# Kernel optimization log

Measured on AMD Instinct MI355X. Metric: run time of the kernel, lower is better.

Reference implementation:

```python
import jax, jax.numpy as jnp
import numpy as np

N, E = 3200, 50000
RBF, HID = 16, 128
CUT = 5.0
NS, NV = 32, 16            # multiplicities of 0e and 1o blocks
D = NS + 3 * NV            # 80 = node/message irrep dim
WNUM = NS*NS + NV*NS + NS*NV + NV*NV  # 2304 tensor-product weights per edge
EPS = 1e-8
# path normalization (fully-connected TP, 2 paths per output irrep)
A1 = 1.0 / np.sqrt(2.0 * NS)
A2 = 1.0 / np.sqrt(2.0 * NV)
A3 = 1.0 / np.sqrt(2.0 * NS)
A4 = 1.0 / np.sqrt(2.0 * NV)
ISQ3 = 1.0 / np.sqrt(3.0)


def setup_inputs() -> dict:
    key = jax.random.key(0)
    ks = jax.random.split(key, 24)
    nrm = lambda k, s, sc=1.0: jax.random.normal(k, s, jnp.float32) * sc
    x = nrm(ks[0], (N, D))
    edge_src = jax.random.randint(ks[1], (E,), 0, N)
    edge_dst = jax.random.randint(ks[2], (E,), 0, N)
    dirs = nrm(ks[3], (E, 3))
    unit = dirs / jnp.linalg.norm(dirs, axis=1, keepdims=True)
    # component-normalized SH for l=0,1: [1, sqrt(3)*r_hat]
    edge_sh = jnp.concatenate([jnp.ones((E, 1), jnp.float32), np.sqrt(3.0) * unit], axis=1)
    edge_rbf = nrm(ks[4], (E, RBF))
    edge_len = jax.random.uniform(ks[5], (E,), jnp.float32, 0.1, 6.0)  # some beyond cutoff
    inp = dict(x=x, edge_src=edge_src, edge_dst=edge_dst, edge_sh=edge_sh,
               edge_rbf=edge_rbf, edge_len=edge_len)
    # IrrepNorm affine params
    inp['norm_w'] = jnp.ones((D,), jnp.float32)
    inp['norm_b'] = jnp.zeros((D,), jnp.float32)
    # radial weight MLP (RBF -> HID -> HID -> WNUM)
    inp['mw1'] = nrm(ks[6], (RBF, HID), 1.0/np.sqrt(RBF)); inp['mb1'] = jnp.zeros((HID,), jnp.float32)
    inp['mw2'] = nrm(ks[7], (HID, HID), 1.0/np.sqrt(HID)); inp['mb2'] = jnp.zeros((HID,), jnp.float32)
    inp['mw3'] = nrm(ks[8], (HID, WNUM), 1.0/np.sqrt(HID)); inp['mb3'] = jnp.zeros((WNUM,), jnp.float32)
    # edge gate MLP (RBF -> HID -> 1)
    inp['gw1'] = nrm(ks[9], (RBF, HID), 1.0/np.sqrt(RBF)); inp['gb1'] = jnp.zeros((HID,), jnp.float32)
    inp['gw2'] = nrm(ks[10], (HID, 1), 1.0/np.sqrt(HID)); inp['gb2'] = jnp.zeros((1,), jnp.float32)
    # equivariant linears (e3nn stores N(0,1) weights, normalizes by 1/sqrt(fan_in))
    inp['Ws'] = nrm(ks[11], (NS, NS + NV))   # msg_linear scalar part: 32 -> 32 scalars + 16 gates
    inp['Wv'] = nrm(ks[12], (NV, NV))        # msg_linear vector part
    inp['Us'] = nrm(ks[13], (NS, NS))        # update_linear
    inp['Uv'] = nrm(ks[14], (NV, NV))
    inp['Ss'] = nrm(ks[15], (NS, NS))        # self_linear
    inp['Sv'] = nrm(ks[16], (NV, NV))
    inp['res_scale'] = jnp.float32(0.1)
    return inp


def _irrep_norm(x, w, b):
    s = x[:, :NS]
    v = x[:, NS:].reshape(-1, NV, 3)
    mean = s.mean(axis=1, keepdims=True)
    var = ((s - mean) ** 2).mean(axis=1, keepdims=True)
    s = (s - mean) / jnp.sqrt(var + EPS)
    rms = jnp.sqrt((v ** 2).mean(axis=2, keepdims=True) + EPS)
    v = v / rms
    out = jnp.concatenate([s, v.reshape(-1, 3 * NV)], axis=-1)
    return out * w + b


def reference(x, edge_src, edge_dst, edge_sh, edge_rbf, edge_len,
              norm_w, norm_b, mw1, mb1, mw2, mb2, mw3, mb3,
              gw1, gb1, gw2, gb2, Ws, Wv, Us, Uv, Ss, Sv, res_scale):
    silu = jax.nn.silu
    x_norm = _irrep_norm(x, norm_w, norm_b)                  # [N, 80]
    # radial tensor-product weights per edge
    h = silu(edge_rbf @ mw1 + mb1)
    h = silu(h @ mw2 + mb2)
    tpw = h @ mw3 + mb3                                      # [E, 2304]
    o1 = NS*NS; o2 = o1 + NV*NS; o3 = o2 + NS*NV
    w1 = tpw[:, :o1].reshape(-1, NS, NS)
    w2 = tpw[:, o1:o2].reshape(-1, NV, NS)
    w3 = tpw[:, o2:o3].reshape(-1, NS, NV)
    w4 = tpw[:, o3:].reshape(-1, NV, NV)
    # gather source node features
    xs = x_norm[edge_src, :NS]                               # [E, 32]
    xv = x_norm[edge_src, NS:].reshape(-1, NV, 3)            # [E, 16, 3]
    sh0 = edge_sh[:, 0]                                      # [E]
    sh1 = edge_sh[:, 1:4]                                    # [E, 3]
    # fully-connected TP paths
    msg_s = A1 * jnp.einsum('ei,eio->eo', xs * sh0[:, None], w1)
    inner = jnp.einsum('eim,em->ei', xv, sh1) * ISQ3         # 1o x 1o -> 0e
    msg_s = msg_s + A2 * jnp.einsum('ei,eio->eo', inner, w2)
    msg_v = A3 * jnp.einsum('ei,eio->eo', xs, w3)[:, :, None] * sh1[:, None, :]
    msg_v = msg_v + A4 * jnp.einsum('eim,eio->eom', xv, w4) * sh0[:, None, None]
    m = jnp.concatenate([msg_s, msg_v.reshape(-1, 3 * NV)], axis=-1)  # [E, 80]
    # cutoff envelope and learned edge gate
    cutoff_w = 0.5 * (jnp.cos(jnp.pi * edge_len / CUT) + 1.0) * (edge_len <= CUT).astype(x.dtype)
    gate_w = jax.nn.sigmoid(silu(edge_rbf @ gw1 + gb1) @ gw2 + gb2)   # [E, 1]
    edge_w = cutoff_w[:, None] * gate_w                               # [E, 1]
    m = m * edge_w
    # scatter-add aggregate + normalization
    agg = jax.ops.segment_sum(m, edge_dst, num_segments=N)            # [N, 80]
    den = jax.ops.segment_sum(edge_w, edge_dst, num_segments=N)       # [N, 1]
    agg = agg / jnp.maximum(den, 1e-8)
    # msg_linear -> scalars + gates + gated vectors
    ag_s = agg[:, :NS]
    ag_v = agg[:, NS:].reshape(-1, NV, 3)
    sc = (ag_s @ Ws) / np.sqrt(NS)                                    # [N, 48]
    vc = jnp.einsum('nim,io->nom', ag_v, Wv) / np.sqrt(NV)            # [N, 16, 3]
    s_g = silu(sc[:, :NS])
    gates = jax.nn.sigmoid(sc[:, NS:])
    v_g = vc * gates[:, :, None]
    # update + self interaction
    upd_s = (s_g @ Us) / np.sqrt(NS)
    upd_v = jnp.einsum('nim,io->nom', v_g, Uv) / np.sqrt(NV)
    self_s = (x_norm[:, :NS] @ Ss) / np.sqrt(NS)
    self_v = jnp.einsum('nim,io->nom', x_norm[:, NS:].reshape(-1, NV, 3), Sv) / np.sqrt(NV)
    out = jnp.concatenate([self_s + upd_s, (self_v + upd_v).reshape(-1, 3 * NV)], axis=-1)
    return x + res_scale * out
```

## Files before the change

kernel.cpp:

```cpp
#include <hip/hip_runtime.h>
#include <hip/hip_bf16.h>
#include <math.h>

#define N_NODES 3200
#define E_EDGES 50000
#define RBFN 16
#define HID 128
#define NS 32
#define NV 16
#define DD 80
#define WNUM 2304
#define CUTF 5.0f
#define EPSF 1e-8f

#define A1C 0.125f
#define A2C 0.17677669529663687f
#define A3C 0.125f
#define A4C 0.17677669529663687f
#define A2ISQ 0.10206207261596575f

typedef __attribute__((ext_vector_type(4))) float f32x4;
typedef __attribute__((ext_vector_type(8))) short bf16x8;

__device__ __forceinline__ float sigm(float x) { return 1.0f / (1.0f + __expf(-x)); }
__device__ __forceinline__ float silu_f(float x) { return x * sigm(x); }

__device__ __forceinline__ short bf16r(float x) {
    union { float f; unsigned u; } v; v.f = x;
    unsigned r = (v.u + 0x7fffu + ((v.u >> 16) & 1u)) >> 16;
    return (short)r;
}
__device__ __forceinline__ float b2f(unsigned short s) {
    union { float f; unsigned u; } v; v.u = ((unsigned)s) << 16; return v.f;
}

__global__ __launch_bounds__(256) void k_pre(
    const int* __restrict__ edst, int* __restrict__ start,
    const float* __restrict__ mw2, __hip_bfloat16* __restrict__ mw2f,
    const float* __restrict__ mw3, const float* __restrict__ mb3,
    __hip_bfloat16* __restrict__ mw3f, __hip_bfloat16* __restrict__ biasf,
    const float* __restrict__ x, const float* __restrict__ nw, const float* __restrict__ nb,
    float* __restrict__ xn, unsigned short* __restrict__ xnb) {
    __shared__ __align__(16) char sm[16640];
    int b = blockIdx.x, t = threadIdx.x;
    if (b == 0) {
        int* histl = (int*)sm;
        int* part  = (int*)(sm + 12800);
        for (int i = t; i < N_NODES; i += 256) histl[i] = 0;
        __syncthreads();
        for (int i = t; i < E_EDGES; i += 256) atomicAdd(&histl[edst[i]], 1);
        __syncthreads();
        int loc[13];
        int s = 0;
#pragma unroll
        for (int j = 0; j < 13; j++) {
            int idx = t * 13 + j;
            int v = (idx < N_NODES) ? histl[idx] : 0;
            loc[j] = s; s += v;
        }
        part[t] = s;
        __syncthreads();
        for (int off = 1; off < 256; off <<= 1) {
            int v = part[t];
            int add = (t >= off) ? part[t - off] : 0;
            __syncthreads();
            part[t] = v + add;
            __syncthreads();
        }
        int pre = (t == 0) ? 0 : part[t - 1];
#pragma unroll
        for (int j = 0; j < 13; j++) {
            int idx = t * 13 + j;
            if (idx < N_NODES) start[idx] = pre + loc[j];
        }
        if (t == 255) start[N_NODES] = part[255];
    } else if (b < 9) {
        __hip_bfloat16* st = (__hip_bfloat16*)sm;
        int tt = b - 1;
        for (int idx = t; idx < 2048; idx += 256) {
            int k = idx >> 4, c = idx & 15;
            float v = mw2[k * HID + tt * 16 + c];
            int kk = k >> 5, q4 = (k >> 3) & 3, j = k & 7;
            st[kk * 512 + (q4 * 16 + c) * 8 + j] = __float2bfloat16(v);
        }
        __syncthreads();
        ((bf16x8*)(mw2f + tt * 2048))[t] = ((const bf16x8*)st)[t];
    } else if (b < 154) {
        int b2 = b - 9;
        __hip_bfloat16* st = (__hip_bfloat16*)sm;
        if (b2 < 144) {
            for (int idx = t; idx < 2048; idx += 256) {
                int k = idx >> 4, c = idx & 15;
                float v = mw3[k * WNUM + b2 * 16 + c];
                int kk = k >> 5, q4 = (k >> 3) & 3, j = k & 7;
                st[kk * 512 + (q4 * 16 + c) * 8 + j] = __float2bfloat16(v);
            }
            __syncthreads();
            ((bf16x8*)(mw3f + b2 * 2048))[t] = ((const bf16x8*)st)[t];
        } else {
            for (int idx = t; idx < 3072; idx += 256) {
                float val;
                if (idx < 1024) {
                    int oh = idx >> 9, l = (idx >> 3) & 63, j = idx & 7;
                    int o = oh * 16 + (l & 15), i = (l >> 4) * 8 + j;
                    val = mb3[i * 32 + o];
                } else if (idx < 2048) {
                    int tt = idx - 1024;
                    int oh = tt >> 9, l = (tt >> 3) & 63, j = tt & 7;
                    int o = oh * 16 + (l & 15), i = (l >> 4) * 8 + j;
                    val = (i < 16) ? mb3[1024 + i * 32 + o] : 0.f;
                } else if (idx < 2560) {
                    int tt = idx - 2048;
                    int l = tt >> 3, j = tt & 7;
                    int o = l & 15, i = (l >> 4) * 8 + j;
                    val = mb3[1536 + i * 16 + o];
                } else {
                    int tt = idx - 2560;
                    int l = tt >> 3, j = tt & 7;
                    int o = l & 15, i = (l >> 4) * 8 + j;
                    val = (i < 16) ? mb3[2048 + i * 16 + o] : 0.f;
                }
                biasf[idx] = __float2bfloat16(val);
            }
        }
    } else {
        float* row = (float*)sm;
        int sub = t >> 6, tt = t & 63;
        int n = (b - 154) * 4 + sub;
        float* rw = row + sub * 80;
        const float* xr = x + n * DD;
        rw[tt] = xr[tt];
        if (tt < 16) rw[64 + tt] = xr[64 + tt];
        __syncthreads();
        float mean = 0.f;
#pragma unroll
        for (int i = 0; i < NS; i++) mean += rw[i];
        mean *= (1.0f / NS);
        float var = 0.f;
#pragma unroll
        for (int i = 0; i < NS; i++) { float d = rw[i] - mean; var += d * d; }
        var *= (1.0f / NS);
        float inv_ = rsqrtf(var + EPSF);
        if (tt < NS) {
            float v = (rw[tt] - mean) * inv_ * nw[tt] + nb[tt];
            xn[n * DD + tt] = v;
            xnb[n * DD + tt] = (unsigned short)bf16r(v);
        }
        if (tt < 48) {
            int j = tt / 3;
            float v0 = rw[NS + 3 * j], v1 = rw[NS + 3 * j + 1], v2 = rw[NS + 3 * j + 2];
            float rms = sqrtf((v0 * v0 + v1 * v1 + v2 * v2) * (1.0f / 3.0f) + EPSF);
            float v = rw[NS + tt] / rms * nw[NS + tt] + nb[NS + tt];
            xn[n * DD + NS + tt] = v;
            xnb[n * DD + NS + tt] = (unsigned short)bf16r(v);
        }
    }
}

__global__ void k_scatter(const int* __restrict__ edst, const int* __restrict__ esrc,
                          const float* __restrict__ esh, const int* __restrict__ start,
                          int* __restrict__ cur, int* __restrict__ inv,
                          int* __restrict__ edstp, int* __restrict__ esrcp,
                          float* __restrict__ eshp) {
    int e = blockIdx.x * 256 + threadIdx.x;
    if (e < E_EDGES) {
        int d = edst[e];
        int pos = start[d] + atomicAdd(&cur[d], 1);
        inv[e] = pos;
        edstp[pos] = d;
        esrcp[pos] = esrc[e];
        f32x4 s = *(const f32x4*)(esh + e * 4);
        *(f32x4*)(eshp + pos * 4) = s;
    }
}

__global__ __launch_bounds__(256) void k_front(
    const float* __restrict__ rbf, const float* __restrict__ elen,
    const int* __restrict__ inv,
    const float* __restrict__ mw1, const float* __restrict__ mb1,
    const float* __restrict__ gw1, const float* __restrict__ gb1,
    const float* __restrict__ gw2, const float* __restrict__ gb2,
    const float* __restrict__ mb2, const __hip_bfloat16* __restrict__ mw2f,
    float* __restrict__ ewg, unsigned short* __restrict__ h2p) {
    __shared__ __align__(16) char smem[16640];
    int b = blockIdx.x, tid = threadIdx.x;
    __hip_bfloat16* h1l = (__hip_bfloat16*)smem;
    float* gatep = (float*)(smem + 16384);
    int wid = __builtin_amdgcn_readfirstlane(tid >> 6);
    int lane = tid & 63;
    int base = b * 64;
    int eb = base + wid * 16;
    {
        int c0 = lane, c1 = 64 + lane;
        float t0[16], t1[16], g0[16], g1[16];
        float b0 = mb1[c0], b1 = mb1[c1], gb0v = gb1[c0], gb1v = gb1[c1];
#pragma unroll
        for (int e = 0; e < 16; e++) { t0[e] = b0; t1[e] = b1; g0[e] = gb0v; g1[e] = gb1v; }
#pragma unroll
        for (int r = 0; r < RBFN; r++) {
            float w0 = mw1[r * HID + c0], w1 = mw1[r * HID + c1];
            float v0 = gw1[r * HID + c0], v1 = gw1[r * HID + c1];
#pragma unroll
            for (int e = 0; e < 16; e++) {
                int ee = eb + e; if (ee >= E_EDGES) ee = E_EDGES - 1;
                float rv = rbf[ee * RBFN + r];
                t0[e] += rv * w0; t1[e] += rv * w1;
                g0[e] += rv * v0; g1[e] += rv * v1;
            }
        }
        float q0 = gw2[c0], q1 = gw2[c1];
        float gb2v = gb2[0];
#pragma unroll
        for (int e = 0; e < 16; e++) {
            int le = wid * 16 + e;
            h1l[le * 128 + c0] = __float2bfloat16(silu_f(t0[e]));
            h1l[le * 128 + c1] = __float2bfloat16(silu_f(t1[e]));
            float p = silu_f(g0[e]) * q0 + silu_f(g1[e]) * q1;
            p += __shfl_xor(p, 1);  p += __shfl_xor(p, 2);  p += __shfl_xor(p, 4);
            p += __shfl_xor(p, 8);  p += __shfl_xor(p, 16); p += __shfl_xor(p, 32);
            if (lane == 0) gatep[le] = p + gb2v;
        }
    }
    __syncthreads();
    if (lane < 16) {
        int ee = eb + lane;
        if (ee < E_EDGES) {
            float len = elen[ee];
            float cut = (len <= CUTF) ? 0.5f * (cosf(3.14159265358979f * len / CUTF) + 1.0f) : 0.f;
            ewg[inv[ee]] = cut * sigm(gatep[wid * 16 + lane]);
        }
    }
    {
        int q4 = lane >> 4, l15 = lane & 15;
        int le = wid * 16 + l15;
        bf16x8 af[4];
#pragma unroll
        for (int kk = 0; kk < 4; kk++)
            af[kk] = *(const bf16x8*)(h1l + le * 128 + kk * 32 + q4 * 8);
        int pos4[4];
#pragma unroll
        for (int r = 0; r < 4; r++) {
            int ge = base + wid * 16 + q4 * 4 + r;
            pos4[r] = (ge < E_EDGES) ? inv[ge] : -1;
        }
        const f32x4 zf = {0.f, 0.f, 0.f, 0.f};
#pragma unroll
        for (int ct = 0; ct < 8; ct++) {
            f32x4 acc = zf;
#pragma unroll
            for (int kk = 0; kk < 4; kk++) {
                bf16x8 bw = *(const bf16x8*)(mw2f + (ct * 4 + kk) * 512 + lane * 8);
                acc = __builtin_amdgcn_mfma_f32_16x16x32_bf16(af[kk], bw, acc, 0, 0, 0);
            }
            float bias = mb2[ct * 16 + l15];
            int c = ct * 16 + l15;
            int f = c >> 3, j = c & 7;
#pragma unroll
            for (int r = 0; r < 4; r++) {
                int pos = pos4[r];
                if (pos >= 0)
                    h2p[(pos >> 4) * 2048 + f * 128 + (pos & 15) * 8 + j] =
                        (unsigned short)bf16r(silu_f(acc[r] + bias));
            }
        }
    }
}

__global__ __launch_bounds__(128, 2) void k_msg(
    const unsigned short* __restrict__ xnb, const unsigned short* __restrict__ h2p,
    const float* __restrict__ ewg, const int* __restrict__ edstp,
    const int* __restrict__ esrcp, const float* __restrict__ eshp,
    const __hip_bfloat16* __restrict__ mw3f, const __hip_bfloat16* __restrict__ biasf,
    const int* __restrict__ startp, float* __restrict__ agg, float* __restrict__ agg2,
    float* __restrict__ den) {
    __shared__ __align__(16) char pool[30720];
    unsigned short (*xng)[88]  = (unsigned short(*)[88])(pool);
    unsigned short (*innr)[16] = (unsigned short(*)[16])(pool + 22528);
    float* sh0l = (float*)(pool + 26624);
    int* srcl   = (int*)(pool + 27136);
    int* dstl   = (int*)(pool + 27648);
    float* ewl  = (float*)(pool + 28160);
    float (*sh1l)[4] = (float(*)[4])(pool + 28672);
    float* msgl = (float*)pool;

    const int tid = threadIdx.x;
    const int wid = __builtin_amdgcn_readfirstlane(tid >> 6);
    const int lane = tid & 63;
    const int q4 = lane >> 4;
    const int l15 = lane & 15;
    const int ib = q4 * 8;
    const int xcd = blockIdx.x & 7;
    const int j8 = blockIdx.x >> 3;
    const int grp = xcd + 8 * (j8 / 5);
    const int slice = j8 - 5 * (j8 / 5);
    if (grp >= 391) return;
    const int e0 = grp * 128;

    {
        int slot = e0 + tid;
        bool v = slot < E_EDGES;
        dstl[tid] = v ? edstp[slot] : -1;
        srcl[tid] = v ? esrcp[slot] : 0;
        ewl[tid]  = v ? ewg[slot] : 0.f;
        f32x4 s = {0.f, 0.f, 0.f, 0.f};
        if (v) s = *(const f32x4*)(eshp + slot * 4);
        sh0l[tid] = s[0];
        sh1l[tid][0] = s[1]; sh1l[tid][1] = s[2]; sh1l[tid][2] = s[3];
    }
    __syncthreads();
    if (slice < 2) {
        for (int idx = tid; idx < 128 * 4; idx += 128) {
            int e = idx >> 2, q = (idx & 3) * 8;
            *(bf16x8*)&xng[e][q] = *(const bf16x8*)(xnb + srcl[e] * 80 + q);
        }
    } else if (slice < 4) {
        for (int idx = tid; idx < 128 * 7; idx += 128) {
            int e = idx / 7, q = 24 + (idx - e * 7) * 8;
            *(bf16x8*)&xng[e][q] = *(const bf16x8*)(xnb + srcl[e] * 80 + q);
        }
    } else {
        for (int idx = tid; idx < 128 * 10; idx += 128) {
            int e = idx / 10, q = (idx - e * 10) * 8;
            *(bf16x8*)&xng[e][q] = *(const bf16x8*)(xnb + srcl[e] * 80 + q);
        }
    }
    __syncthreads();
    if (slice == 2 || slice == 3) {
        for (int idx = tid; idx < 128 * 16; idx += 128) {
            int e = idx >> 4, i = idx & 15;
            float d = b2f(xng[e][32 + 3 * i]) * sh1l[e][0]
                    + b2f(xng[e][32 + 3 * i + 1]) * sh1l[e][1]
                    + b2f(xng[e][32 + 3 * i + 2]) * sh1l[e][2];
            innr[e][i] = (unsigned short)bf16r(A2ISQ * d);
        }
        __syncthreads();
    }

    int el[4];
#pragma unroll
    for (int et = 0; et < 4; et++) el[et] = wid * 64 + et * 16 + l15;
    const int tbase = (e0 >> 4) + wid * 4;
    bf16x8 hfr[4][4];
#pragma unroll
    for (int et = 0; et < 4; et++) {
        const unsigned short* tp = h2p + (tbase + et) * 2048;
#pragma unroll
        for (int kk = 0; kk < 4; kk++)
            hfr[et][kk] = *(const bf16x8*)(tp + (kk * 4 + q4) * 128 + l15 * 8);
    }
    const f32x4 zf = {0.f, 0.f, 0.f, 0.f};
    const bf16x8* gp = (const bf16x8*)mw3f;
    int cnt = E_EDGES - e0; if (cnt > 128) cnt = 128;

    if (slice < 4) {
        const int h = slice & 1;
        const int ch2 = slice >> 1;
        const int nlo = ch2 * 24, nhi = nlo + 24;
        float f1[4];
        f32x4 msgS[4];
#pragma unroll
        for (int et = 0; et < 4; et++) f1[et] = A1C * sh0l[el[et]];
#pragma unroll
        for (int et = 0; et < 4; et++) {
            bf16x8 pb;
            if (ch2 == 0) {
#pragma unroll
                for (int j = 0; j < 8; j++)
                    pb[j] = bf16r(b2f(xng[el[et]][ib + j]) * f1[et]);
            } else {
#pragma unroll
                for (int j = 0; j < 8; j++)
                    pb[j] = (ib + j < 16) ? (short)innr[el[et]][ib + j] : (short)0;
            }
            bf16x8 ba = *(const bf16x8*)(biasf + (ch2 * 1024 + h * 512) + lane * 8);
            msgS[et] = __builtin_amdgcn_mfma_f32_16x16x32_bf16(ba, pb, zf, 0, 0, 0);
        }
        auto computeS = [&](int n, bf16x8 (&A)[4]) {
            f32x4 acc[4];
#pragma unroll
            for (int et = 0; et < 4; et++) acc[et] = zf;
#pragma unroll
            for (int kk = 0; kk < 4; kk++)
#pragma unroll
                for (int et = 0; et < 4; et++)
                    acc[et] = __builtin_amdgcn_mfma_f32_16x16x32_bf16(
                        A[kk], hfr[et][kk], acc[et], 0, 0, 0);
            float p[4];
            if (n < 32) {
#pragma unroll
                for (int et = 0; et < 4; et++) p[et] = f1[et] * b2f(xng[el[et]][n]);
            } else {
#pragma unroll
                for (int et = 0; et < 4; et++) p[et] = b2f(innr[el[et]][n - 32]);
            }
#pragma unroll
            for (int et = 0; et < 4; et++)
#pragma unroll
                for (int r = 0; r < 4; r++)
                    msgS[et][r] += p[et] * acc[et][r];
        };
        bf16x8 A0[4], A1[4];
        {
            const bf16x8* g = gp + nlo * 512 + h * 256;
#pragma unroll
            for (int f = 0; f < 4; f++) A0[f] = g[f * 64 + lane];
        }
        for (int n = nlo; n < nhi; n += 2) {
            const bf16x8* g1 = gp + (n + 1) * 512 + h * 256;
#pragma unroll
            for (int f = 0; f < 4; f++) A1[f] = g1[f * 64 + lane];
            computeS(n, A0);
            if (n + 2 < nhi) {
                const bf16x8* g2 = gp + (n + 2) * 512 + h * 256;
#pragma unroll
                for (int f = 0; f < 4; f++) A0[f] = g2[f * 64 + lane];
            }
            computeS(n + 1, A1);
        }
        __syncthreads();
#pragma unroll
        for (int et = 0; et < 4; et++) {
            int le = el[et];
            float ew = ewl[le];
#pragma unroll
            for (int r = 0; r < 4; r++)
                msgl[le * 16 + q4 * 4 + r] = msgS[et][r] * ew;
        }
        __syncthreads();
        {
            int nch = (slice == 0) ? 17 : 16;
            int c = lane;
            int r0 = wid * 64;
            int rend = (cnt < r0 + 64) ? cnt : (r0 + 64);
            if (c < nch && r0 < cnt) {
                int cur = dstl[r0];
                float acc = 0.f;
                for (int r = r0; r < rend; r++) {
                    int nd = dstl[r];
                    if (nd != cur) {
                        if (cur >= 0) {
                            bool interior = (startp[cur] >= e0 + r0) && (startp[cur + 1] <= e0 + rend);
                            float* p = (c == 16) ? (den + cur)
                                     : ((slice == 0) ? (agg + cur * 80 + c)
                                     :  (slice == 1) ? (agg + cur * 80 + 16 + c)
                                     :  (slice == 2) ? (agg2 + cur * 32 + c)
                                                     : (agg2 + cur * 32 + 16 + c));
                            if (interior) *p = acc; else atomicAdd(p, acc);
                        }
                        acc = 0.f; cur = nd;
                    }
                    acc += (c == 16) ? ewl[r] : msgl[r * 16 + c];
                }
                if (cur >= 0) {
                    bool interior = (startp[cur] >= e0 + r0) && (startp[cur + 1] <= e0 + rend);
                    float* p = (c == 16) ? (den + cur)
                             : ((slice == 0) ? (agg + cur * 80 + c)
                             :  (slice == 1) ? (agg + cur * 80 + 16 + c)
                             :  (slice == 2) ? (agg2 + cur * 32 + c)
                                             : (agg2 + cur * 32 + 16 + c));
                    if (interior) *p = acc; else atomicAdd(p, acc);
                }
            }
        }
    } else {
        float f4e[4];
#pragma unroll
        for (int et = 0; et < 4; et++) f4e[et] = A4C * sh0l[el[et]];
        f32x4 q3[4];
#pragma unroll
        for (int et = 0; et < 4; et++) {
            bf16x8 xs8;
#pragma unroll
            for (int j = 0; j < 8; j++) xs8[j] = (short)xng[el[et]][ib + j];
            bf16x8 ba3 = *(const bf16x8*)(biasf + 2048 + lane * 8);
            q3[et] = __builtin_amdgcn_mfma_f32_16x16x32_bf16(ba3, xs8, zf, 0, 0, 0);
        }
        for (int n = 48; n < 64; ++n) {
            bf16x8 A[8];
            const bf16x8* g = gp + n * 512;
#pragma unroll
            for (int f = 0; f < 8; f++) A[f] = g[f * 64 + lane];
#pragma unroll
            for (int half = 0; half < 2; half++) {
                f32x4 acc[4];
#pragma unroll
                for (int et = 0; et < 4; et++) acc[et] = zf;
#pragma unroll
                for (int kk = 0; kk < 4; kk++)
#pragma unroll
                    for (int et = 0; et < 4; et++)
                        acc[et] = __builtin_amdgcn_mfma_f32_16x16x32_bf16(
                            A[half * 4 + kk], hfr[et][kk], acc[et], 0, 0, 0);
                int i = 2 * (n - 48) + half;
                float p[4];
#pragma unroll
                for (int et = 0; et < 4; et++) p[et] = b2f(xng[el[et]][i]);
#pragma unroll
                for (int et = 0; et < 4; et++)
#pragma unroll
                    for (int r = 0; r < 4; r++)
                        q3[et][r] += p[et] * acc[et][r];
            }
        }
        f32x4 qv[3][4];
#pragma unroll
        for (int et = 0; et < 4; et++) {
            bf16x8 ba4 = *(const bf16x8*)(biasf + 2560 + lane * 8);
#pragma unroll
            for (int m = 0; m < 3; m++) {
                bf16x8 t8;
#pragma unroll
                for (int j = 0; j < 8; j++) {
                    int i = ib + j;
                    t8[j] = (i < 16) ? (short)xng[el[et]][32 + 3 * i + m] : (short)0;
                }
                qv[m][et] = __builtin_amdgcn_mfma_f32_16x16x32_bf16(ba4, t8, zf, 0, 0, 0);
            }
        }
        for (int n = 64; n < 72; ++n) {
            bf16x8 A[8];
            const bf16x8* g = gp + n * 512;
#pragma unroll
            for (int f = 0; f < 8; f++) A[f] = g[f * 64 + lane];
#pragma unroll
            for (int half = 0; half < 2; half++) {
                f32x4 acc[4];
#pragma unroll
                for (int et = 0; et < 4; et++) acc[et] = zf;
#pragma unroll
                for (int kk = 0; kk < 4; kk++)
#pragma unroll
                    for (int et = 0; et < 4; et++)
                        acc[et] = __builtin_amdgcn_mfma_f32_16x16x32_bf16(
                            A[half * 4 + kk], hfr[et][kk], acc[et], 0, 0, 0);
                int i = 2 * (n - 64) + half;
#pragma unroll
                for (int m = 0; m < 3; m++) {
                    float p[4];
#pragma unroll
                    for (int et = 0; et < 4; et++) p[et] = b2f(xng[el[et]][32 + 3 * i + m]);
#pragma unroll
                    for (int et = 0; et < 4; et++)
#pragma unroll
                        for (int r = 0; r < 4; r++)
                            qv[m][et][r] += p[et] * acc[et][r];
                }
            }
        }
        __syncthreads();
#pragma unroll
        for (int et = 0; et < 4; et++) {
            int le = el[et];
            float ew = ewl[le];
            float s0 = sh1l[le][0], s1 = sh1l[le][1], s2 = sh1l[le][2];
            float b4 = f4e[et];
#pragma unroll
            for (int r = 0; r < 4; r++) {
                int o = q4 * 4 + r;
                float qq = A3C * q3[et][r];
                msgl[le * 48 + o * 3 + 0] = (qq * s0 + b4 * qv[0][et][r]) * ew;
                msgl[le * 48 + o * 3 + 1] = (qq * s1 + b4 * qv[1][et][r]) * ew;
                msgl[le * 48 + o * 3 + 2] = (qq * s2 + b4 * qv[2][et][r]) * ew;
            }
        }
        __syncthreads();
        {
            int c = lane;
            int r0 = wid * 64;
            int rend = (cnt < r0 + 64) ? cnt : (r0 + 64);
            if (c < 48 && r0 < cnt) {
                int cur = dstl[r0];
                float acc = 0.f;
                for (int r = r0; r < rend; r++) {
                    int nd = dstl[r];
                    if (nd != cur) {
                        if (cur >= 0) {
                            bool interior = (startp[cur] >= e0 + r0) && (startp[cur + 1] <= e0 + rend);
                            float* p = agg + cur * 80 + 32 + c;
                            if (interior) *p = acc; else atomicAdd(p, acc);
                        }
                        acc = 0.f; cur = nd;
                    }
                    acc += msgl[r * 48 + c];
                }
                if (cur >= 0) {
                    bool interior = (startp[cur] >= e0 + r0) && (startp[cur + 1] <= e0 + rend);
                    float* p = agg + cur * 80 + 32 + c;
                    if (interior) *p = acc; else atomicAdd(p, acc);
                }
            }
        }
    }
}

__global__ __launch_bounds__(256) void k_update(
    const float* __restrict__ x, const float* __restrict__ xn,
    const float* __restrict__ agg, const float* __restrict__ agg2,
    const float* __restrict__ den,
    const float* __restrict__ Ws, const float* __restrict__ Wv,
    const float* __restrict__ Us, const float* __restrict__ Uv,
    const float* __restrict__ Ss, const float* __restrict__ Sv,
    const float* __restrict__ rsp, float* __restrict__ out) {
    int sub = threadIdx.x >> 6, t = threadIdx.x & 63;
    int n = blockIdx.x * 4 + sub;
    __shared__ float ag[4][DD];
    __shared__ float xnl[4][DD];
    __shared__ float sg[4][NS];
    __shared__ float gt[4][NV];
    __shared__ float vg[4][48];
    float idv = 1.0f / fmaxf(den[n], 1e-8f);
    float base = agg[n * DD + t];
    if (t < 32) base += agg2[n * 32 + t];
    ag[sub][t] = base * idv;
    if (t < 16) ag[sub][64 + t] = agg[n * DD + 64 + t] * idv;
    xnl[sub][t] = xn[n * DD + t];
    if (t < 16) xnl[sub][64 + t] = xn[n * DD + 64 + t];
    __syncthreads();
    const float iqs = 0.17677669529663687f;
    const float iqv = 0.25f;
    if (t < 48) {
        float acc = 0.f;
#pragma unroll
        for (int i = 0; i < NS; i++) acc += ag[sub][i] * Ws[i * 48 + t];
        acc *= iqs;
        if (t < NS) sg[sub][t] = silu_f(acc);
        else gt[sub][t - NS] = sigm(acc);
    }
    __syncthreads();
    if (t < 48) {
        int o = t / 3, m = t - 3 * o;
        float acc = 0.f;
#pragma unroll
        for (int i = 0; i < NV; i++) acc += ag[sub][NS + 3 * i + m] * Wv[i * NV + o];
        vg[sub][t] = acc * iqv * gt[sub][o];
    }
    __syncthreads();
    float rs = rsp[0];
    if (t < NS) {
        float us = 0.f, ss = 0.f;
#pragma unroll
        for (int i = 0; i < NS; i++) { us += sg[sub][i] * Us[i * NS + t]; ss += xnl[sub][i] * Ss[i * NS + t]; }
        out[n * DD + t] = x[n * DD + t] + rs * ((ss + us) * iqs);
    }
    if (t < 48) {
        int o = t / 3, m = t - 3 * o;
        float uv = 0.f, sv = 0.f;
#pragma unroll
        for (int i = 0; i < NV; i++) { uv += vg[sub][3 * i + m] * Uv[i * NV + o]; sv += xnl[sub][NS + 3 * i + m] * Sv[i * NV + o]; }
        out[n * DD + NS + t] = x[n * DD + NS + t] + rs * ((sv + uv) * iqv);
    }
}

extern "C" void kernel_launch(void* const* d_in, const int* in_sizes, int n_in,
                              void* d_out, int out_size, void* d_ws, size_t ws_size,
                              hipStream_t stream) {
    (void)in_sizes; (void)n_in; (void)out_size; (void)ws_size;
    const float* x    = (const float*)d_in[0];
    const int*   esrc = (const int*)d_in[1];
    const int*   edst = (const int*)d_in[2];
    const float* esh  = (const float*)d_in[3];
    const float* erbf = (const float*)d_in[4];
    const float* elen = (const float*)d_in[5];
    const float* nw   = (const float*)d_in[6];
    const float* nb   = (const float*)d_in[7];
    const float* mw1  = (const float*)d_in[8];
    const float* mb1  = (const float*)d_in[9];
    const float* mw2  = (const float*)d_in[10];
    const float* mb2  = (const float*)d_in[11];
    const float* mw3  = (const float*)d_in[12];
    const float* mb3  = (const float*)d_in[13];
    const float* gw1  = (const float*)d_in[14];
    const float* gb1  = (const float*)d_in[15];
    const float* gw2  = (const float*)d_in[16];
    const float* gb2  = (const float*)d_in[17];
    const float* Ws   = (const float*)d_in[18];
    const float* Wv   = (const float*)d_in[19];
    const float* Us   = (const float*)d_in[20];
    const float* Uv   = (const float*)d_in[21];
    const float* Ss   = (const float*)d_in[22];
    const float* Sv   = (const float*)d_in[23];
    const float* rsp  = (const float*)d_in[24];
    float* out = (float*)d_out;
    float* ws  = (float*)d_ws;

    float* agg    = ws;
    float* den    = ws + 256000;
    float* agg2   = ws + 259200;
    int*   cur    = (int*)(ws + 361600);
    int*   startp = (int*)(ws + 368000);
    int*   inv    = (int*)(ws + 371204);
    float* xn     = ws + 421204;
    float* ewg    = ws + 677204;
    unsigned short* h2p = (unsigned short*)(ws + 727204);
    __hip_bfloat16* mw3f  = (__hip_bfloat16*)(ws + 3930276);
    __hip_bfloat16* biasf = (__hip_bfloat16*)(ws + 4077732);
    __hip_bfloat16* mw2f  = (__hip_bfloat16*)(ws + 4079268);
    int* edstp    = (int*)(ws + 4087460);
    int* esrcp    = (int*)(ws + 4137508);
    float* eshp   = ws + 4187556;
    unsigned short* xnb = (unsigned short*)(ws + 4387748);

    hipMemsetAsync(ws, 0, 364800 * sizeof(float), stream);
    k_pre<<<954, 256, 0, stream>>>(edst, startp, mw2, mw2f, mw3, mb3, mw3f, biasf,
                                   x, nw, nb, xn, xnb);
    k_scatter<<<196, 256, 0, stream>>>(edst, esrc, esh, startp, cur,
                                       inv, edstp, esrcp, eshp);
    k_front<<<782, 256, 0, stream>>>(erbf, elen, inv, mw1, mb1, gw1, gb1, gw2, gb2,
                                     mb2, mw2f, ewg, h2p);
    k_msg<<<1960, 128, 0, stream>>>(xnb, h2p, ewg, edstp, esrcp, eshp,
                                    mw3f, biasf, startp, agg, agg2, den);
    k_update<<<800, 256, 0, stream>>>(x, xn, agg, agg2, den, Ws, Wv, Us, Uv, Ss, Sv, rsp, out);
}
```

Baseline: 272.8 us.

## Parallelize destination histogram across blocks and split scan into separate kernel

The degree histogram used to be built by a single block looping over all 50k edges with shared-memory atomics, which serialized the prep kernel's critical path. It is now computed by 196 blocks with global atomics into a zeroed workspace buffer. A new small kernel does the prefix scan and also the mw2 bf16 repacking. This adds one kernel launch and global atomic contention, and frees shared memory in k_pre.

```diff
diff --git a/kernel.cpp b/kernel.cpp
--- a/kernel.cpp
+++ b/kernel.cpp
@@ -35,58 +35,18 @@
 }
 
 __global__ __launch_bounds__(256) void k_pre(
-    const int* __restrict__ edst, int* __restrict__ start,
-    const float* __restrict__ mw2, __hip_bfloat16* __restrict__ mw2f,
+    const int* __restrict__ edst, int* __restrict__ hist,
     const float* __restrict__ mw3, const float* __restrict__ mb3,
     __hip_bfloat16* __restrict__ mw3f, __hip_bfloat16* __restrict__ biasf,
     const float* __restrict__ x, const float* __restrict__ nw, const float* __restrict__ nb,
     float* __restrict__ xn, unsigned short* __restrict__ xnb) {
-    __shared__ __align__(16) char sm[16640];
+    __shared__ __align__(16) char sm[4096];
     int b = blockIdx.x, t = threadIdx.x;
-    if (b == 0) {
-        int* histl = (int*)sm;
-        int* part  = (int*)(sm + 12800);
-        for (int i = t; i < N_NODES; i += 256) histl[i] = 0;
-        __syncthreads();
-        for (int i = t; i < E_EDGES; i += 256) atomicAdd(&histl[edst[i]], 1);
-        __syncthreads();
-        int loc[13];
-        int s = 0;
-#pragma unroll
-        for (int j = 0; j < 13; j++) {
-            int idx = t * 13 + j;
-            int v = (idx < N_NODES) ? histl[idx] : 0;
-            loc[j] = s; s += v;
-        }
-        part[t] = s;
-        __syncthreads();
-        for (int off = 1; off < 256; off <<= 1) {
-            int v = part[t];
-            int add = (t >= off) ? part[t - off] : 0;
-            __syncthreads();
-            part[t] = v + add;
-            __syncthreads();
-        }
-        int pre = (t == 0) ? 0 : part[t - 1];
-#pragma unroll
-        for (int j = 0; j < 13; j++) {
-            int idx = t * 13 + j;
-            if (idx < N_NODES) start[idx] = pre + loc[j];
-        }
-        if (t == 255) start[N_NODES] = part[255];
-    } else if (b < 9) {
-        __hip_bfloat16* st = (__hip_bfloat16*)sm;
-        int tt = b - 1;
-        for (int idx = t; idx < 2048; idx += 256) {
-            int k = idx >> 4, c = idx & 15;
-            float v = mw2[k * HID + tt * 16 + c];
-            int kk = k >> 5, q4 = (k >> 3) & 3, j = k & 7;
-            st[kk * 512 + (q4 * 16 + c) * 8 + j] = __float2bfloat16(v);
-        }
-        __syncthreads();
-        ((bf16x8*)(mw2f + tt * 2048))[t] = ((const bf16x8*)st)[t];
-    } else if (b < 154) {
-        int b2 = b - 9;
+    if (b < 196) {
+        int e = b * 256 + t;
+        if (e < E_EDGES) atomicAdd(&hist[edst[e]], 1);
+    } else if (b < 341) {
+        int b2 = b - 196;
         __hip_bfloat16* st = (__hip_bfloat16*)sm;
         if (b2 < 144) {
             for (int idx = t; idx < 2048; idx += 256) {
@@ -124,10 +84,10 @@
             }
         }
     } else {
-        float* row = (float*)sm;
+        __shared__ __align__(16) float row[4][80];
         int sub = t >> 6, tt = t & 63;
-        int n = (b - 154) * 4 + sub;
-        float* rw = row + sub * 80;
+        int n = (b - 341) * 4 + sub;
+        float* rw = row[sub];
         const float* xr = x + n * DD;
         rw[tt] = xr[tt];
         if (tt < 16) rw[64 + tt] = xr[64 + tt];
@@ -154,6 +114,50 @@
             xn[n * DD + NS + tt] = v;
             xnb[n * DD + NS + tt] = (unsigned short)bf16r(v);
         }
+    }
+}
+
+__global__ void k_scan_prep(const int* __restrict__ hist, int* __restrict__ start,
+                            const float* __restrict__ mw2, __hip_bfloat16* __restrict__ mw2f) {
+    __shared__ __align__(16) char sm[4096];
+    int b = blockIdx.x, t = threadIdx.x;
+    if (b == 0) {
+        int* part = (int*)sm;
+        int loc[13];
+        int s = 0;
+#pragma unroll
+        for (int j = 0; j < 13; j++) {
+            int idx = t * 13 + j;
+            int v = (idx < N_NODES) ? hist[idx] : 0;
+            loc[j] = s; s += v;
+        }
+        part[t] = s;
+        __syncthreads();
+        for (int off = 1; off < 256; off <<= 1) {
+            int v = part[t];
+            int add = (t >= off) ? part[t - off] : 0;
+            __syncthreads();
+            part[t] = v + add;
+            __syncthreads();
+        }
+        int pre = (t == 0) ? 0 : part[t - 1];
+#pragma unroll
+        for (int j = 0; j < 13; j++) {
+            int idx = t * 13 + j;
+            if (idx < N_NODES) start[idx] = pre + loc[j];
+        }
+        if (t == 255) start[N_NODES] = part[255];
+    } else {
+        __hip_bfloat16* st = (__hip_bfloat16*)sm;
+        int tt = b - 1;
+        for (int idx = t; idx < 2048; idx += 256) {
+            int k = idx >> 4, c = idx & 15;
+            float v = mw2[k * HID + tt * 16 + c];
+            int kk = k >> 5, q4 = (k >> 3) & 3, j = k & 7;
+            st[kk * 512 + (q4 * 16 + c) * 8 + j] = __float2bfloat16(v);
+        }
+        __syncthreads();
+        ((bf16x8*)(mw2f + tt * 2048))[t] = ((const bf16x8*)st)[t];
     }
 }
 
@@ -686,7 +690,8 @@
     float* agg    = ws;
     float* den    = ws + 256000;
     float* agg2   = ws + 259200;
-    int*   cur    = (int*)(ws + 361600);
+    int*   hist   = (int*)(ws + 361600);
+    int*   cur    = (int*)(ws + 364800);
     int*   startp = (int*)(ws + 368000);
     int*   inv    = (int*)(ws + 371204);
     float* xn     = ws + 421204;
@@ -700,9 +705,10 @@
     float* eshp   = ws + 4187556;
     unsigned short* xnb = (unsigned short*)(ws + 4387748);
 
-    hipMemsetAsync(ws, 0, 364800 * sizeof(float), stream);
-    k_pre<<<954, 256, 0, stream>>>(edst, startp, mw2, mw2f, mw3, mb3, mw3f, biasf,
-                                   x, nw, nb, xn, xnb);
+    hipMemsetAsync(ws, 0, 368000 * sizeof(float), stream);
+    k_pre<<<1141, 256, 0, stream>>>(edst, hist, mw3, mb3, mw3f, biasf,
+                                    x, nw, nb, xn, xnb);
+    k_scan_prep<<<9, 256, 0, stream>>>(hist, startp, mw2, mw2f);
     k_scatter<<<196, 256, 0, stream>>>(edst, esrc, esh, startp, cur,
                                        inv, edstp, esrcp, eshp);
     k_front<<<782, 256, 0, stream>>>(erbf, elen, inv, mw1, mb1, gw1, gb1, gw2, gb2,
```

After: 234.1 us. 1.17x faster.
